# Performance work log

Measured on AMD Instinct MI355X. Metric: run time of the kernel, lower is better.

Reference implementation:

```python
import math
import jax, jax.numpy as jnp
import numpy as np

B = 256          # graphs per batch
N0 = 512         # nodes per graph
DEG = 16         # avg degree
E = B * N0 * DEG # total edges
F_IN = 160
H = 64
RATIO = 0.11
NUM_CLASSES = 2


def setup_inputs() -> dict:
    key = jax.random.key(0)
    ks = jax.random.split(key, 20)
    x = jax.random.normal(ks[0], (B * N0, F_IN), jnp.float32)
    # within-graph random edges: src/dst local in [0, N0) plus graph offset
    eg = E // B
    off = (jnp.arange(B, dtype=jnp.int32) * N0)[:, None]
    src = (jax.random.randint(ks[1], (B, eg), 0, N0, jnp.int32) + off).reshape(-1)
    dst = (jax.random.randint(ks[2], (B, eg), 0, N0, jnp.int32) + off).reshape(-1)
    edge_index = jnp.stack([src, dst], 0)
    s = lambda fan: 1.0 / np.sqrt(fan)
    inp = {
        'x': x,
        'edge_index': edge_index,
        'conv1_Wr': jax.random.normal(ks[3], (F_IN, H), jnp.float32) * s(F_IN),
        'conv1_Wl': jax.random.normal(ks[4], (F_IN, H), jnp.float32) * s(F_IN),
        'conv1_b': jnp.zeros((H,), jnp.float32),
        'convs_Wr': jax.random.normal(ks[5], (5, H, H), jnp.float32) * s(H),
        'convs_Wl': jax.random.normal(ks[6], (5, H, H), jnp.float32) * s(H),
        'convs_b': jnp.zeros((5, H), jnp.float32),
        'pools_Wr': jax.random.normal(ks[7], (2, H, 1), jnp.float32) * s(H),
        'pools_Wl': jax.random.normal(ks[8], (2, H, 1), jnp.float32) * s(H),
        'pools_b': jnp.zeros((2, 1), jnp.float32),
        'lin1_W': jax.random.normal(ks[9], (6 * H, H), jnp.float32) * s(6 * H),
        'lin1_b': jnp.zeros((H,), jnp.float32),
        'lin2_W': jax.random.normal(ks[10], (H, NUM_CLASSES), jnp.float32) * s(H),
        'lin2_b': jnp.zeros((NUM_CLASSES,), jnp.float32),
    }
    return inp


def _gconv(x, src, dst, emask, Wr, Wl, b, n_nodes):
    # PyG GraphConv(aggr='mean'): lin_rel(mean_{j->i} x_j) + lin_root(x)
    msg = x[src] * emask[:, None]                              # [E, F]
    agg = jax.ops.segment_sum(msg, dst, num_segments=n_nodes)  # [N, F]
    deg = jax.ops.segment_sum(emask, dst, num_segments=n_nodes)
    agg = agg / jnp.maximum(deg, 1.0)[:, None]
    return agg @ Wr + b + x @ Wl


def _sag_pool(x, src, dst, emask, Wr, Wl, b, n_per, k):
    n_nodes = B * n_per
    score = _gconv(x, src, dst, emask, Wr, Wl, b, n_nodes)[:, 0]   # [N]
    _, idx = jax.lax.top_k(score.reshape(B, n_per), k)             # [B, k]
    perm = (idx + (jnp.arange(B, dtype=jnp.int32) * n_per)[:, None]).reshape(-1)
    new_x = x[perm] * jnp.tanh(score[perm])[:, None]
    newpos = jnp.full((n_nodes,), -1, jnp.int32).at[perm].set(
        jnp.arange(B * k, dtype=jnp.int32))
    ns, nd = newpos[src], newpos[dst]
    valid = (ns >= 0) & (nd >= 0)
    new_emask = emask * valid.astype(emask.dtype)
    return new_x, jnp.where(valid, ns, 0), jnp.where(valid, nd, 0), new_emask


def _gmp(x, n_per):  # global_mean_pool with equal-size graphs
    return x.reshape(B, n_per, -1).mean(axis=1)


def reference(x, edge_index, conv1_Wr, conv1_Wl, conv1_b, convs_Wr, convs_Wl,
              convs_b, pools_Wr, pools_Wl, pools_b, lin1_W, lin1_b,
              lin2_W, lin2_b):
    src, dst = edge_index[0], edge_index[1]
    emask = jnp.ones(src.shape, x.dtype)
    n = N0
    x = jax.nn.relu(_gconv(x, src, dst, emask, conv1_Wr, conv1_Wl, conv1_b, B * n))
    xs = [_gmp(x, n)]
    for i in range(5):
        x = jax.nn.relu(_gconv(x, src, dst, emask, convs_Wr[i], convs_Wl[i],
                               convs_b[i], B * n))
        xs.append(_gmp(x, n))
        if i % 2 == 0 and i < 4:
            j = i // 2
            k = math.ceil(RATIO * n)
            x, src, dst, emask = _sag_pool(x, src, dst, emask, pools_Wr[j],
                                           pools_Wl[j], pools_b[j], n, k)
            n = k
    h = jnp.concatenate(xs, axis=-1)          # JumpingKnowledge('cat') -> [B, 6H]
    h = jax.nn.relu(h @ lin1_W + lin1_b)
    h = h @ lin2_W + lin2_b                   # dropout is identity in eval mode
    return jax.nn.log_softmax(h, axis=-1)
```

## Files before the change

### kernel.cpp

```cpp
#include <hip/hip_runtime.h>
#include <math.h>

namespace {
constexpr int NB   = 256;
constexpr int EPG  = 8192;
constexpr int ETOT = NB * EPG;
constexpr int FH   = 64;
constexpr int NN0  = NB * 512;
}

__device__ float g_feat[3][(size_t)NN0 * FH];
__device__ float g_xs[NB * 6 * FH];
__device__ int   g_esrc[2][ETOT];
__device__ int   g_edst[2][ETOT];
__device__ int   g_ecnt[2][NB];
__device__ unsigned short g_csr[ETOT];
__device__ unsigned int   g_deg[NN0], g_start[NN0];

template<int K>
__global__ __launch_bounds__(256)
void mm_dual(const float* __restrict__ xext, int in_idx,
             const float* __restrict__ Wr, const float* __restrict__ Wl,
             const float* __restrict__ bias, int zr_idx, int xl_idx)
{
  constexpr int RPB = 64;
  constexpr int KC  = 32;
  __shared__ float xs[RPB][KC];
  __shared__ float wrT[KC/4][64][4];
  __shared__ float wlT[KC/4][64][4];
  const float* __restrict__ x = (in_idx < 0) ? xext : g_feat[in_idx];
  float* __restrict__ zr = g_feat[zr_idx];
  float* __restrict__ xl = g_feat[xl_idx];
  const int t = threadIdx.x;
  const int rowbase = blockIdx.x * RPB;
  const int f  = t & 31;
  const int rg = t >> 5;
  const int wv = t >> 6;
  const int wc = t & 63;
  const int wq = t >> 6;
  float ar0[8], ar1[8], al0[8], al1[8];
  #pragma unroll
  for (int r = 0; r < 8; ++r) { ar0[r]=0.f; ar1[r]=0.f; al0[r]=0.f; al1[r]=0.f; }

  for (int c = 0; c < K / KC; ++c) {
    __syncthreads();
    #pragma unroll
    for (int i = 0; i < 2; ++i) {
      const int idx = t + i * 256;
      const int r = idx >> 3, q = idx & 7;
      const float* gp = &x[(size_t)(rowbase + r) * K + c * KC + q * 4];
      float* lp = &xs[0][0] + (size_t)(i * 256 + wv * 64) * 4;
      __builtin_amdgcn_global_load_lds(
          (const __attribute__((address_space(1))) unsigned int*)gp,
          (__attribute__((address_space(3))) unsigned int*)lp, 16, 0, 0);
    }
    #pragma unroll
    for (int h = 0; h < 2; ++h) {
      const int kq = wq * 2 + h;
      #pragma unroll
      for (int i = 0; i < 4; ++i) {
        const int krow = c * KC + kq * 4 + i;
        wrT[kq][wc][i] = Wr[(size_t)krow * 64 + wc];
        wlT[kq][wc][i] = Wl[(size_t)krow * 64 + wc];
      }
    }
    __syncthreads();
    for (int k4 = 0; k4 < KC / 4; ++k4) {
      const float4 wr0 = *reinterpret_cast<const float4*>(&wrT[k4][f][0]);
      const float4 wr1 = *reinterpret_cast<const float4*>(&wrT[k4][f+32][0]);
      const float4 wl0 = *reinterpret_cast<const float4*>(&wlT[k4][f][0]);
      const float4 wl1 = *reinterpret_cast<const float4*>(&wlT[k4][f+32][0]);
      #pragma unroll
      for (int r = 0; r < 8; ++r) {
        const float4 xv = *reinterpret_cast<const float4*>(&xs[rg*8 + r][k4*4]);
        float a0 = ar0[r], a1 = ar1[r], b0 = al0[r], b1 = al1[r];
        a0 = fmaf(xv.x, wr0.x, a0); a0 = fmaf(xv.y, wr0.y, a0);
        a0 = fmaf(xv.z, wr0.z, a0); a0 = fmaf(xv.w, wr0.w, a0);
        a1 = fmaf(xv.x, wr1.x, a1); a1 = fmaf(xv.y, wr1.y, a1);
        a1 = fmaf(xv.z, wr1.z, a1); a1 = fmaf(xv.w, wr1.w, a1);
        b0 = fmaf(xv.x, wl0.x, b0); b0 = fmaf(xv.y, wl0.y, b0);
        b0 = fmaf(xv.z, wl0.z, b0); b0 = fmaf(xv.w, wl0.w, b0);
        b1 = fmaf(xv.x, wl1.x, b1); b1 = fmaf(xv.y, wl1.y, b1);
        b1 = fmaf(xv.z, wl1.z, b1); b1 = fmaf(xv.w, wl1.w, b1);
        ar0[r] = a0; ar1[r] = a1; al0[r] = b0; al1[r] = b1;
      }
    }
  }
  const float bv0 = bias[f], bv1 = bias[f + 32];
  #pragma unroll
  for (int r = 0; r < 8; ++r) {
    const size_t row = (size_t)(rowbase + rg * 8 + r);
    zr[row * 64 + f]      = ar0[r];
    zr[row * 64 + f + 32] = ar1[r];
    xl[row * 64 + f]      = al0[r] + bv0;
    xl[row * 64 + f + 32] = al1[r] + bv1;
  }
}

__global__ __launch_bounds__(1024)
void agg_full_build(int zr_idx, int xl_idx,
                    const int* __restrict__ esrc, const int* __restrict__ edst,
                    int out_idx, int xs_off)
{
  __shared__ float zlds[512 * 64];
  __shared__ unsigned short csr[EPG];
  __shared__ unsigned int hist[512], bufA[512], bufB[512];
  __shared__ float red[16][64];
  const float* __restrict__ zr  = g_feat[zr_idx];
  const float* __restrict__ xlb = g_feat[xl_idx];
  float* __restrict__ xout = g_feat[out_idx];
  const int g = blockIdx.x, t = threadIdx.x;
  const int gbase = g * 512, ebase = g * EPG;
  if (t < 512) hist[t] = 0;
  __syncthreads();
  {
    const float4* zsrc = reinterpret_cast<const float4*>(zr + (size_t)gbase * 64);
    float4* zdst = reinterpret_cast<float4*>(zlds);
    #pragma unroll
    for (int i = 0; i < 8; ++i) zdst[t + i * 1024] = zsrc[t + i * 1024];
  }
  for (int e = t; e < EPG; e += 1024)
    atomicAdd(&hist[edst[ebase + e] - gbase], 1u);
  __syncthreads();
  if (t < 512) bufA[t] = hist[t];
  __syncthreads();
  unsigned int *pa = bufA, *pb = bufB;
  for (int off = 1; off < 512; off <<= 1) {
    if (t < 512) {
      unsigned int v = pa[t];
      if (t >= off) v += pa[t - off];
      pb[t] = v;
    }
    __syncthreads();
    unsigned int* tmp = pa; pa = pb; pb = tmp;
  }
  unsigned int excl = 0;
  if (t < 512) excl = pa[t] - hist[t];
  __syncthreads();
  if (t < 512) { bufA[t] = excl; bufB[t] = excl; }
  __syncthreads();
  for (int e = t; e < EPG; e += 1024) {
    const int sl = esrc[ebase + e] - gbase;
    const int dl = edst[ebase + e] - gbase;
    const unsigned int pos = atomicAdd(&bufB[dl], 1u);
    csr[pos] = (unsigned short)sl;
  }
  __syncthreads();
  if (t < 512) { g_deg[gbase + t] = hist[t]; g_start[gbase + t] = bufA[t]; }
  {
    unsigned int* gcsr32 = reinterpret_cast<unsigned int*>(&g_csr[ebase]);
    const unsigned int* lcsr32 = reinterpret_cast<const unsigned int*>(csr);
    for (int i = t; i < EPG/2; i += 1024) gcsr32[i] = lcsr32[i];
  }
  const int lane = t & 63, w = t >> 6;
  float psum = 0.f;
  for (int nd = w; nd < 512; nd += 16) {
    const unsigned int s = bufA[nd], d = hist[nd];
    float a0 = 0.f, a1 = 0.f, a2 = 0.f, a3 = 0.f;
    unsigned int j = 0;
    for (; j + 4 <= d; j += 4) {
      const int i0 = csr[s+j], i1 = csr[s+j+1], i2 = csr[s+j+2], i3 = csr[s+j+3];
      a0 += zlds[i0*64 + lane]; a1 += zlds[i1*64 + lane];
      a2 += zlds[i2*64 + lane]; a3 += zlds[i3*64 + lane];
    }
    for (; j < d; ++j) a0 += zlds[csr[s+j]*64 + lane];
    const float acc = (a0 + a1) + (a2 + a3);
    float v = acc / (float)(d > 0 ? d : 1) + xlb[(size_t)(gbase + nd)*64 + lane];
    v = fmaxf(v, 0.f);
    xout[(size_t)(gbase + nd)*64 + lane] = v;
    psum += v;
  }
  red[w][lane] = psum;
  __syncthreads();
  if (t < 64) {
    float s = 0.f;
    #pragma unroll
    for (int ww = 0; ww < 16; ++ww) s += red[ww][t];
    g_xs[g*384 + xs_off + t] = s * (1.f/512.f);
  }
}

__global__ __launch_bounds__(1024)
void agg_full_use(int zr_idx, int xl_idx, int out_idx, int xs_off)
{
  __shared__ float zlds[512 * 64];
  __shared__ unsigned short csr[EPG];
  __shared__ unsigned int hist[512], start[512];
  __shared__ float red[16][64];
  const float* __restrict__ zr  = g_feat[zr_idx];
  const float* __restrict__ xlb = g_feat[xl_idx];
  float* __restrict__ xout = g_feat[out_idx];
  const int g = blockIdx.x, t = threadIdx.x;
  const int gbase = g * 512, ebase = g * EPG;
  if (t < 512) { hist[t] = g_deg[gbase + t]; start[t] = g_start[gbase + t]; }
  {
    const float4* zsrc = reinterpret_cast<const float4*>(zr + (size_t)gbase * 64);
    float4* zdst = reinterpret_cast<float4*>(zlds);
    #pragma unroll
    for (int i = 0; i < 8; ++i) zdst[t + i * 1024] = zsrc[t + i * 1024];
  }
  {
    const uint4* c4 = reinterpret_cast<const uint4*>(&g_csr[ebase]);
    uint4* l4 = reinterpret_cast<uint4*>(csr);
    l4[t] = c4[t];
  }
  __syncthreads();
  const int lane = t & 63, w = t >> 6;
  float psum = 0.f;
  for (int nd = w; nd < 512; nd += 16) {
    const unsigned int s = start[nd], d = hist[nd];
    float a0 = 0.f, a1 = 0.f, a2 = 0.f, a3 = 0.f;
    unsigned int j = 0;
    for (; j + 4 <= d; j += 4) {
      const int i0 = csr[s+j], i1 = csr[s+j+1], i2 = csr[s+j+2], i3 = csr[s+j+3];
      a0 += zlds[i0*64 + lane]; a1 += zlds[i1*64 + lane];
      a2 += zlds[i2*64 + lane]; a3 += zlds[i3*64 + lane];
    }
    for (; j < d; ++j) a0 += zlds[csr[s+j]*64 + lane];
    const float acc = (a0 + a1) + (a2 + a3);
    float v = acc / (float)(d > 0 ? d : 1) + xlb[(size_t)(gbase + nd)*64 + lane];
    v = fmaxf(v, 0.f);
    xout[(size_t)(gbase + nd)*64 + lane] = v;
    psum += v;
  }
  red[w][lane] = psum;
  __syncthreads();
  if (t < 64) {
    float s = 0.f;
    #pragma unroll
    for (int ww = 0; ww < 16; ++ww) s += red[ww][t];
    g_xs[g*384 + xs_off + t] = s * (1.f/512.f);
  }
}

__global__ __launch_bounds__(512)
void sag_pool0(int in_idx,
               const int* __restrict__ esrc, const int* __restrict__ edst,
               const float* __restrict__ wr, const float* __restrict__ wl,
               const float* __restrict__ pb,
               int xnew_idx, int out_stage)
{
  constexpr int NPER = 512, NPOW2 = 512, KSEL = 57;
  __shared__ float zs[NPER], swl[NPER], sscore[NPER];
  __shared__ unsigned long long keys[NPOW2];
  __shared__ unsigned short pcsr[EPG];
  __shared__ short newpos[NPER];
  __shared__ int scnt;
  const float* __restrict__ xin = g_feat[in_idx];
  float* __restrict__ xnew = g_feat[xnew_idx];
  int* __restrict__ eosrc = g_esrc[out_stage];
  int* __restrict__ eodst = g_edst[out_stage];
  const int g = blockIdx.x, t = threadIdx.x;
  const int gbase = g * NPER, ebase = g * EPG;
  const int lane = t & 63, w = t >> 6;
  const float wrv = wr[lane], wlv = wl[lane];
  for (int nd = w; nd < NPER; nd += 8) {
    const float v = xin[(size_t)(gbase + nd)*64 + lane];
    float a = v * wrv, b = v * wlv;
    #pragma unroll
    for (int off = 32; off > 0; off >>= 1) {
      a += __shfl_xor(a, off);
      b += __shfl_xor(b, off);
    }
    if (lane == 0) { zs[nd] = a; swl[nd] = b; }
  }
  {
    const unsigned int* gcsr32 = reinterpret_cast<const unsigned int*>(&g_csr[ebase]);
    unsigned int* lcsr32 = reinterpret_cast<unsigned int*>(pcsr);
    for (int i = t; i < EPG/2; i += 512) lcsr32[i] = gcsr32[i];
  }
  if (t == 0) scnt = 0;
  __syncthreads();
  if (t < NPER) {
    const unsigned int s = g_start[gbase + t], d = g_deg[gbase + t];
    float a = 0.f;
    for (unsigned int j = 0; j < d; ++j) a += zs[pcsr[s + j]];
    sscore[t] = a / fmaxf((float)d, 1.f) + pb[0] + swl[t];
  }
  __syncthreads();
  if (t < NPOW2) {
    unsigned long long key = 0ull;
    if (t < NPER) {
      unsigned int u = __float_as_uint(sscore[t]);
      u = (u & 0x80000000u) ? ~u : (u | 0x80000000u);
      key = ((unsigned long long)u << 32) | (unsigned int)(~(unsigned int)t);
    }
    keys[t] = key;
  }
  __syncthreads();
  for (int kk = 2; kk <= NPOW2; kk <<= 1) {
    for (int j = kk >> 1; j > 0; j >>= 1) {
      if (t < NPOW2) {
        const int ixj = t ^ j;
        if (ixj > t) {
          const unsigned long long a = keys[t], bk = keys[ixj];
          const bool up = ((t & kk) == 0);
          if (up ? (a < bk) : (a > bk)) { keys[t] = bk; keys[ixj] = a; }
        }
      }
      __syncthreads();
    }
  }
  if (t < NPER) newpos[t] = -1;
  __syncthreads();
  if (t < KSEL)
    newpos[(int)(~(unsigned int)(keys[t] & 0xffffffffull))] = (short)t;
  __syncthreads();
  for (int r = w; r < KSEL; r += 8) {
    const int old = (int)(~(unsigned int)(keys[r] & 0xffffffffull));
    const float sc = tanhf(sscore[old]);
    xnew[(size_t)(g*KSEL + r)*64 + lane] =
        xin[(size_t)(gbase + old)*64 + lane] * sc;
  }
  for (int e = t; e < EPG; e += 512) {
    const int sl = esrc[ebase + e] - gbase;
    const int dl = edst[ebase + e] - gbase;
    const int ns = newpos[sl], nd2 = newpos[dl];
    if (ns >= 0 && nd2 >= 0) {
      const int slot = atomicAdd(&scnt, 1);
      eosrc[ebase + slot] = g*KSEL + ns;
      eodst[ebase + slot] = g*KSEL + nd2;
    }
  }
  __syncthreads();
  if (t == 0) g_ecnt[out_stage][g] = scnt;
}

__device__ __forceinline__ void conv_small(
    float* X, float* Z, float* ACC, float* w_s, const float* deg,
    const float* Wr, const float* Wl, const float* bias,
    int n, const int* esrc, const int* edst, int m, int gb, int ebase,
    int xs_off, int g, int t, int lane, int w)
{
  for (int i = t; i < n*64; i += 512) { Z[i] = 0.f; ACC[i] = 0.f; }
  __syncthreads();
  for (int kc = 0; kc < 4; ++kc) {
    for (int i = t; i < 1024; i += 512) w_s[i] = Wr[kc*1024 + i];
    __syncthreads();
    for (int r = w; r < n; r += 8) {
      float zacc = 0.f;
      #pragma unroll
      for (int k = 0; k < 16; ++k)
        zacc = fmaf(X[r*64 + kc*16 + k], w_s[k*64 + lane], zacc);
      Z[r*64 + lane] += zacc;
    }
    __syncthreads();
  }
  for (int e = w; e < m; e += 8) {
    const int sl = esrc[ebase + e] - gb;
    const int dl = edst[ebase + e] - gb;
    atomicAdd(&ACC[dl*64 + lane], Z[sl*64 + lane]);
  }
  __syncthreads();
  for (int i = t; i < n*64; i += 512) {
    const int r = i >> 6, f = i & 63;
    Z[i] = ACC[i] / fmaxf(deg[r], 1.f) + bias[f];
  }
  __syncthreads();
  for (int kc = 0; kc < 4; ++kc) {
    for (int i = t; i < 1024; i += 512) w_s[i] = Wl[kc*1024 + i];
    __syncthreads();
    for (int r = w; r < n; r += 8) {
      float zacc = 0.f;
      #pragma unroll
      for (int k = 0; k < 16; ++k)
        zacc = fmaf(X[r*64 + kc*16 + k], w_s[k*64 + lane], zacc);
      Z[r*64 + lane] += zacc;
    }
    __syncthreads();
  }
  for (int i = t; i < n*64; i += 512) X[i] = fmaxf(Z[i], 0.f);
  __syncthreads();
  if (t < 64) {
    float s = 0.f;
    for (int r = 0; r < n; ++r) s += X[r*64 + t];
    g_xs[g*384 + xs_off + t] = s / (float)n;
  }
  __syncthreads();
}

__global__ __launch_bounds__(512)
void tail(const float* __restrict__ cWr, const float* __restrict__ cWl,
          const float* __restrict__ cb,
          const float* __restrict__ pWr, const float* __restrict__ pWl,
          const float* __restrict__ pb)
{
  __shared__ float X[57*64], Z[57*64], ACC[57*64];
  __shared__ float w_s[16*64];
  __shared__ float deg[64];
  __shared__ float zs[64], swl[64], sagg[64], sscore[64];
  __shared__ unsigned long long keys[64];
  __shared__ short newpos[64];
  __shared__ int scnt;
  const int g = blockIdx.x, t = threadIdx.x;
  const int lane = t & 63, w = t >> 6;
  const int ebase = g * EPG;

  for (int i = t; i < 57*64; i += 512) X[i] = g_feat[0][(size_t)(g*57)*64 + i];
  const int m0 = g_ecnt[0][g];
  if (t < 64) deg[t] = 0.f;
  __syncthreads();
  for (int e = t; e < m0; e += 512)
    atomicAdd(&deg[g_edst[0][ebase + e] - g*57], 1.f);
  __syncthreads();

  conv_small(X, Z, ACC, w_s, deg, cWr + 4096,  cWl + 4096,  cb + 64,
             57, g_esrc[0], g_edst[0], m0, g*57, ebase, 128, g, t, lane, w);
  conv_small(X, Z, ACC, w_s, deg, cWr + 8192,  cWl + 8192,  cb + 128,
             57, g_esrc[0], g_edst[0], m0, g*57, ebase, 192, g, t, lane, w);

  {
    const float pwrv = pWr[64 + lane], pwlv = pWl[64 + lane];
    for (int r = w; r < 57; r += 8) {
      float a = X[r*64 + lane] * pwrv, b = X[r*64 + lane] * pwlv;
      #pragma unroll
      for (int off = 32; off > 0; off >>= 1) {
        a += __shfl_xor(a, off);
        b += __shfl_xor(b, off);
      }
      if (lane == 0) { zs[r] = a; swl[r] = b; }
    }
    if (t < 64) sagg[t] = 0.f;
    if (t == 0) scnt = 0;
    __syncthreads();
    for (int e = t; e < m0; e += 512)
      atomicAdd(&sagg[g_edst[0][ebase + e] - g*57],
                zs[g_esrc[0][ebase + e] - g*57]);
    __syncthreads();
    if (t < 57) sscore[t] = sagg[t] / fmaxf(deg[t], 1.f) + pb[1] + swl[t];
    __syncthreads();
    if (t < 64) {
      unsigned long long key = 0ull;
      if (t < 57) {
        unsigned int u = __float_as_uint(sscore[t]);
        u = (u & 0x80000000u) ? ~u : (u | 0x80000000u);
        key = ((unsigned long long)u << 32) | (unsigned int)(~(unsigned int)t);
      }
      keys[t] = key;
    }
    __syncthreads();
    for (int kk = 2; kk <= 64; kk <<= 1) {
      for (int j = kk >> 1; j > 0; j >>= 1) {
        if (t < 64) {
          const int ixj = t ^ j;
          if (ixj > t) {
            const unsigned long long a = keys[t], bk = keys[ixj];
            const bool up = ((t & kk) == 0);
            if (up ? (a < bk) : (a > bk)) { keys[t] = bk; keys[ixj] = a; }
          }
        }
        __syncthreads();
      }
    }
    if (t < 64) newpos[t] = -1;
    __syncthreads();
    if (t < 7)
      newpos[(int)(~(unsigned int)(keys[t] & 0xffffffffull))] = (short)t;
    __syncthreads();
    for (int r = w; r < 7; r += 8) {
      const int old = (int)(~(unsigned int)(keys[r] & 0xffffffffull));
      const float sc = tanhf(sscore[old]);
      Z[r*64 + lane] = X[old*64 + lane] * sc;
    }
    for (int e = t; e < m0; e += 512) {
      const int sl = g_esrc[0][ebase + e] - g*57;
      const int dl = g_edst[0][ebase + e] - g*57;
      const int ns = newpos[sl], nd2 = newpos[dl];
      if (ns >= 0 && nd2 >= 0) {
        const int slot = atomicAdd(&scnt, 1);
        g_esrc[1][ebase + slot] = g*7 + ns;
        g_edst[1][ebase + slot] = g*7 + nd2;
      }
    }
    __syncthreads();
    for (int i = t; i < 7*64; i += 512) X[i] = Z[i];
    if (t < 64) deg[t] = 0.f;
    __syncthreads();
  }
  const int m1 = scnt;
  for (int e = t; e < m1; e += 512)
    atomicAdd(&deg[g_edst[1][ebase + e] - g*7], 1.f);
  __syncthreads();

  conv_small(X, Z, ACC, w_s, deg, cWr + 12288, cWl + 12288, cb + 192,
             7, g_esrc[1], g_edst[1], m1, g*7, ebase, 256, g, t, lane, w);
  conv_small(X, Z, ACC, w_s, deg, cWr + 16384, cWl + 16384, cb + 256,
             7, g_esrc[1], g_edst[1], m1, g*7, ebase, 320, g, t, lane, w);
}

__global__ __launch_bounds__(64)
void head(const float* __restrict__ W1, const float* __restrict__ b1,
          const float* __restrict__ W2, const float* __restrict__ b2,
          float* __restrict__ out)
{
  __shared__ float h[384], o1[64], lg[2];
  const int g = blockIdx.x, t = threadIdx.x;
  for (int i = t; i < 384; i += 64) h[i] = g_xs[g*384 + i];
  __syncthreads();
  float acc = b1[t];
  for (int j = 0; j < 384; ++j) acc = fmaf(h[j], W1[j*64 + t], acc);
  o1[t] = fmaxf(acc, 0.f);
  __syncthreads();
  if (t < 2) {
    float a2 = b2[t];
    for (int f2 = 0; f2 < 64; ++f2) a2 = fmaf(o1[f2], W2[f2*2 + t], a2);
    lg[t] = a2;
  }
  __syncthreads();
  if (t < 2) {
    const float mx = fmaxf(lg[0], lg[1]);
    const float lse = mx + logf(expf(lg[0]-mx) + expf(lg[1]-mx));
    out[g*2 + t] = lg[t] - lse;
  }
}

extern "C" void kernel_launch(void* const* d_in, const int* in_sizes, int n_in,
                              void* d_out, int out_size, void* d_ws, size_t ws_size,
                              hipStream_t stream)
{
  (void)in_sizes; (void)n_in; (void)d_ws; (void)ws_size; (void)out_size;
  const float* x    = (const float*)d_in[0];
  const int*   ei   = (const int*)d_in[1];
  const float* c1Wr = (const float*)d_in[2];
  const float* c1Wl = (const float*)d_in[3];
  const float* c1b  = (const float*)d_in[4];
  const float* cWr  = (const float*)d_in[5];
  const float* cWl  = (const float*)d_in[6];
  const float* cb   = (const float*)d_in[7];
  const float* pWr  = (const float*)d_in[8];
  const float* pWl  = (const float*)d_in[9];
  const float* pb   = (const float*)d_in[10];
  const float* l1W  = (const float*)d_in[11];
  const float* l1b  = (const float*)d_in[12];
  const float* l2W  = (const float*)d_in[13];
  const float* l2b  = (const float*)d_in[14];
  float* out = (float*)d_out;
  const int* esrc = ei;
  const int* edst = ei + ETOT;

  mm_dual<160><<<NN0/64, 256, 0, stream>>>(x, -1, c1Wr, c1Wl, c1b, 0, 1);
  agg_full_build<<<NB, 1024, 0, stream>>>(0, 1, esrc, edst, 1, 0);
  mm_dual<64><<<NN0/64, 256, 0, stream>>>(nullptr, 1, cWr, cWl, cb, 0, 2);
  agg_full_use<<<NB, 1024, 0, stream>>>(0, 2, 2, 64);
  sag_pool0<<<NB, 512, 0, stream>>>(2, esrc, edst, pWr, pWl, pb, 0, 0);
  tail<<<NB, 512, 0, stream>>>(cWr, cWl, cb, pWr, pWl, pb);
  head<<<NB, 64, 0, stream>>>(l1W, l1b, l2W, l2b, out);
}
```

Baseline: 372.1 us.

## Fuse second conv matmul into per-graph aggregation kernel; enlarge first matmul tile

```diff
diff --git a/kernel.cpp b/kernel.cpp
--- a/kernel.cpp
+++ b/kernel.cpp
@@ -23,7 +23,7 @@
              const float* __restrict__ Wr, const float* __restrict__ Wl,
              const float* __restrict__ bias, int zr_idx, int xl_idx)
 {
-  constexpr int RPB = 64;
+  constexpr int RPB = 128;
   constexpr int KC  = 32;
   __shared__ float xs[RPB][KC];
   __shared__ float wrT[KC/4][64][4];
@@ -38,14 +38,14 @@
   const int wv = t >> 6;
   const int wc = t & 63;
   const int wq = t >> 6;
-  float ar0[8], ar1[8], al0[8], al1[8];
+  float ar0[16], ar1[16], al0[16], al1[16];
   #pragma unroll
-  for (int r = 0; r < 8; ++r) { ar0[r]=0.f; ar1[r]=0.f; al0[r]=0.f; al1[r]=0.f; }
+  for (int r = 0; r < 16; ++r) { ar0[r]=0.f; ar1[r]=0.f; al0[r]=0.f; al1[r]=0.f; }
 
   for (int c = 0; c < K / KC; ++c) {
     __syncthreads();
     #pragma unroll
-    for (int i = 0; i < 2; ++i) {
+    for (int i = 0; i < 4; ++i) {
       const int idx = t + i * 256;
       const int r = idx >> 3, q = idx & 7;
       const float* gp = &x[(size_t)(rowbase + r) * K + c * KC + q * 4];
@@ -65,14 +65,15 @@
       }
     }
     __syncthreads();
+    #pragma unroll 1
     for (int k4 = 0; k4 < KC / 4; ++k4) {
       const float4 wr0 = *reinterpret_cast<const float4*>(&wrT[k4][f][0]);
       const float4 wr1 = *reinterpret_cast<const float4*>(&wrT[k4][f+32][0]);
       const float4 wl0 = *reinterpret_cast<const float4*>(&wlT[k4][f][0]);
       const float4 wl1 = *reinterpret_cast<const float4*>(&wlT[k4][f+32][0]);
       #pragma unroll
-      for (int r = 0; r < 8; ++r) {
-        const float4 xv = *reinterpret_cast<const float4*>(&xs[rg*8 + r][k4*4]);
+      for (int r = 0; r < 16; ++r) {
+        const float4 xv = *reinterpret_cast<const float4*>(&xs[rg*16 + r][k4*4]);
         float a0 = ar0[r], a1 = ar1[r], b0 = al0[r], b1 = al1[r];
         a0 = fmaf(xv.x, wr0.x, a0); a0 = fmaf(xv.y, wr0.y, a0);
         a0 = fmaf(xv.z, wr0.z, a0); a0 = fmaf(xv.w, wr0.w, a0);
@@ -88,8 +89,8 @@
   }
   const float bv0 = bias[f], bv1 = bias[f + 32];
   #pragma unroll
-  for (int r = 0; r < 8; ++r) {
-    const size_t row = (size_t)(rowbase + rg * 8 + r);
+  for (int r = 0; r < 16; ++r) {
+    const size_t row = (size_t)(rowbase + rg * 16 + r);
     zr[row * 64 + f]      = ar0[r];
     zr[row * 64 + f + 32] = ar1[r];
     xl[row * 64 + f]      = al0[r] + bv0;
@@ -181,33 +182,71 @@
 }
 
 __global__ __launch_bounds__(1024)
-void agg_full_use(int zr_idx, int xl_idx, int out_idx, int xs_off)
+void conv_agg_fused(int x_idx, const float* __restrict__ Wr,
+                    const float* __restrict__ Wl, const float* __restrict__ bias,
+                    int out_idx, int xs_off)
 {
   __shared__ float zlds[512 * 64];
   __shared__ unsigned short csr[EPG];
   __shared__ unsigned int hist[512], start[512];
-  __shared__ float red[16][64];
-  const float* __restrict__ zr  = g_feat[zr_idx];
-  const float* __restrict__ xlb = g_feat[xl_idx];
+  __shared__ float w_r[1024], w_l[1024];
+  const float* __restrict__ X1 = g_feat[x_idx];
   float* __restrict__ xout = g_feat[out_idx];
   const int g = blockIdx.x, t = threadIdx.x;
   const int gbase = g * 512, ebase = g * EPG;
+  const int lane = t & 63, w = t >> 6;
+  {
+    const float4* src = reinterpret_cast<const float4*>(X1 + (size_t)gbase * 64);
+    float4* dst = reinterpret_cast<float4*>(zlds);
+    #pragma unroll
+    for (int i = 0; i < 8; ++i) dst[t + i * 1024] = src[t + i * 1024];
+  }
   if (t < 512) { hist[t] = g_deg[gbase + t]; start[t] = g_start[gbase + t]; }
-  {
-    const float4* zsrc = reinterpret_cast<const float4*>(zr + (size_t)gbase * 64);
-    float4* zdst = reinterpret_cast<float4*>(zlds);
-    #pragma unroll
-    for (int i = 0; i < 8; ++i) zdst[t + i * 1024] = zsrc[t + i * 1024];
-  }
   {
     const uint4* c4 = reinterpret_cast<const uint4*>(&g_csr[ebase]);
     uint4* l4 = reinterpret_cast<uint4*>(csr);
     l4[t] = c4[t];
   }
-  __syncthreads();
-  const int lane = t & 63, w = t >> 6;
+  const int ndbase = w * 32;
+  float zacc[32], xla[32];
+  #pragma unroll
+  for (int i = 0; i < 32; ++i) { zacc[i] = 0.f; xla[i] = 0.f; }
+  #pragma unroll 1
+  for (int c = 0; c < 4; ++c) {
+    __syncthreads();
+    w_r[t] = Wr[c * 1024 + t];
+    w_l[t] = Wl[c * 1024 + t];
+    __syncthreads();
+    #pragma unroll 1
+    for (int k4 = 0; k4 < 4; ++k4) {
+      const int kb = k4 * 4;
+      const float wr0 = w_r[(kb+0)*64 + lane], wr1 = w_r[(kb+1)*64 + lane],
+                  wr2 = w_r[(kb+2)*64 + lane], wr3 = w_r[(kb+3)*64 + lane];
+      const float wl0 = w_l[(kb+0)*64 + lane], wl1 = w_l[(kb+1)*64 + lane],
+                  wl2 = w_l[(kb+2)*64 + lane], wl3 = w_l[(kb+3)*64 + lane];
+      #pragma unroll
+      for (int i = 0; i < 32; ++i) {
+        const float4 xv = *reinterpret_cast<const float4*>(
+            &zlds[(ndbase + i) * 64 + c * 16 + kb]);
+        float za = zacc[i], xa = xla[i];
+        za = fmaf(xv.x, wr0, za); za = fmaf(xv.y, wr1, za);
+        za = fmaf(xv.z, wr2, za); za = fmaf(xv.w, wr3, za);
+        xa = fmaf(xv.x, wl0, xa); xa = fmaf(xv.y, wl1, xa);
+        xa = fmaf(xv.z, wl2, xa); xa = fmaf(xv.w, wl3, xa);
+        zacc[i] = za; xla[i] = xa;
+      }
+    }
+  }
+  __syncthreads();
+  #pragma unroll
+  for (int i = 0; i < 32; ++i)
+    zlds[(ndbase + i) * 64 + lane] = zacc[i];
+  __syncthreads();
+  const float bv = bias[lane];
   float psum = 0.f;
-  for (int nd = w; nd < 512; nd += 16) {
+  #pragma unroll 1
+  for (int i = 0; i < 32; ++i) {
+    const int nd = ndbase + i;
     const unsigned int s = start[nd], d = hist[nd];
     float a0 = 0.f, a1 = 0.f, a2 = 0.f, a3 = 0.f;
     unsigned int j = 0;
@@ -217,18 +256,18 @@
       a2 += zlds[i2*64 + lane]; a3 += zlds[i3*64 + lane];
     }
     for (; j < d; ++j) a0 += zlds[csr[s+j]*64 + lane];
-    const float acc = (a0 + a1) + (a2 + a3);
-    float v = acc / (float)(d > 0 ? d : 1) + xlb[(size_t)(gbase + nd)*64 + lane];
+    float v = ((a0 + a1) + (a2 + a3)) / (float)(d > 0 ? d : 1) + xla[i] + bv;
     v = fmaxf(v, 0.f);
     xout[(size_t)(gbase + nd)*64 + lane] = v;
     psum += v;
   }
-  red[w][lane] = psum;
+  __syncthreads();
+  zlds[w * 64 + lane] = psum;
   __syncthreads();
   if (t < 64) {
     float s = 0.f;
     #pragma unroll
-    for (int ww = 0; ww < 16; ++ww) s += red[ww][t];
+    for (int ww = 0; ww < 16; ++ww) s += zlds[ww*64 + t];
     g_xs[g*384 + xs_off + t] = s * (1.f/512.f);
   }
 }
@@ -538,10 +577,9 @@
   const int* esrc = ei;
   const int* edst = ei + ETOT;
 
-  mm_dual<160><<<NN0/64, 256, 0, stream>>>(x, -1, c1Wr, c1Wl, c1b, 0, 1);
+  mm_dual<160><<<NN0/128, 256, 0, stream>>>(x, -1, c1Wr, c1Wl, c1b, 0, 1);
   agg_full_build<<<NB, 1024, 0, stream>>>(0, 1, esrc, edst, 1, 0);
-  mm_dual<64><<<NN0/64, 256, 0, stream>>>(nullptr, 1, cWr, cWl, cb, 0, 2);
-  agg_full_use<<<NB, 1024, 0, stream>>>(0, 2, 2, 64);
+  conv_agg_fused<<<NB, 1024, 0, stream>>>(1, cWr, cWl, cb, 2, 64);
   sag_pool0<<<NB, 512, 0, stream>>>(2, esrc, edst, pWr, pWl, pb, 0, 0);
   tail<<<NB, 512, 0, stream>>>(cWr, cWl, cb, pWr, pWl, pb);
   head<<<NB, 64, 0, stream>>>(l1W, l1b, l2W, l2b, out);
```

After: 367.5 us. No clear change (-1.3%).
